# Kernel tuning notes

Measured on AMD Instinct MI355X. Metric: run time of the kernel, lower is better.

Reference implementation:

```python
import jax, jax.numpy as jnp
import numpy as np

N_NODES = 100000
N_EDGES = 400000
N_GRAPHS = 4096
F_IN, HID, HEADS, OUT_DIM = 64, 64, 4, 128
NEG_SLOPE = 0.2


def gat_layer(x, src, dst, W, a_s, a_d, b, concat):
    # x: [N, Fin]; W: [Fin, H*C]; a_s/a_d: [H, C]; src/dst: [Etot] (self loops included)
    N = x.shape[0]
    H, C = a_s.shape
    h = (x @ W).reshape(N, H, C)
    e_src = jnp.einsum('nhc,hc->nh', h, a_s)  # [N, H]
    e_dst = jnp.einsum('nhc,hc->nh', h, a_d)
    e = jax.nn.leaky_relu(e_src[src] + e_dst[dst], NEG_SLOPE)  # [Etot, H]
    # segment softmax over edges grouped by destination node
    m = jax.ops.segment_max(e, dst, num_segments=N)
    m = jnp.where(jnp.isfinite(m), m, 0.0)
    ex = jnp.exp(e - m[dst])
    denom = jax.ops.segment_sum(ex, dst, num_segments=N)
    alpha = ex / jnp.maximum(denom[dst], 1e-16)  # [Etot, H]
    out = jax.ops.segment_sum(alpha[:, :, None] * h[src], dst, num_segments=N)  # [N, H, C]
    out = out.reshape(N, H * C) if concat else out.mean(axis=1)
    return out + b


def setup_inputs() -> dict:
    key = jax.random.key(0)
    ks = jax.random.split(key, 32)
    x = jax.random.normal(ks[0], (N_NODES, F_IN), dtype=jnp.float32)
    edge_index = jax.random.randint(ks[1], (2, N_EDGES), 0, N_NODES, dtype=jnp.int64) if jax.config.jax_enable_x64 else jax.random.randint(ks[1], (2, N_EDGES), 0, N_NODES).astype(jnp.int32)
    batch = jnp.sort(jax.random.randint(ks[2], (N_NODES,), 0, N_GRAPHS)).astype(edge_index.dtype)
    s = 0.1
    d = {
        'x': x, 'edge_index': edge_index, 'batch': batch, 'num_graphs': N_GRAPHS,
        'W0': jax.random.normal(ks[3], (F_IN, HEADS * HID), jnp.float32) * s,
        'as0': jax.random.normal(ks[4], (HEADS, HID), jnp.float32) * s,
        'ad0': jax.random.normal(ks[5], (HEADS, HID), jnp.float32) * s,
        'b0': jnp.zeros((HEADS * HID,), jnp.float32),
        'W1': jax.random.normal(ks[6], (HEADS * HID, HEADS * HID), jnp.float32) * s,
        'as1': jax.random.normal(ks[7], (HEADS, HID), jnp.float32) * s,
        'ad1': jax.random.normal(ks[8], (HEADS, HID), jnp.float32) * s,
        'b1': jnp.zeros((HEADS * HID,), jnp.float32),
        'W2': jax.random.normal(ks[9], (HEADS * HID, HEADS * HID), jnp.float32) * s,
        'as2': jax.random.normal(ks[10], (HEADS, HID), jnp.float32) * s,
        'ad2': jax.random.normal(ks[11], (HEADS, HID), jnp.float32) * s,
        'b2': jnp.zeros((HEADS * HID,), jnp.float32),
        'W3': jax.random.normal(ks[12], (HEADS * HID, OUT_DIM), jnp.float32) * s,
        'as3': jax.random.normal(ks[13], (1, OUT_DIM), jnp.float32) * s,
        'ad3': jax.random.normal(ks[14], (1, OUT_DIM), jnp.float32) * s,
        'b3': jnp.zeros((OUT_DIM,), jnp.float32),
        'mW0': jax.random.normal(ks[15], (OUT_DIM, OUT_DIM // 2), jnp.float32) * s,
        'mb0': jnp.zeros((OUT_DIM // 2,), jnp.float32),
        'mW1': jax.random.normal(ks[16], (OUT_DIM // 2, OUT_DIM // 4), jnp.float32) * s,
        'mb1': jnp.zeros((OUT_DIM // 4,), jnp.float32),
        'mW2': jax.random.normal(ks[17], (OUT_DIM // 4, 4), jnp.float32) * s,
        'mb2': jnp.zeros((4,), jnp.float32),
    }
    return d


def reference(x, edge_index, batch, num_graphs, W0, as0, ad0, b0, W1, as1, ad1, b1,
              W2, as2, ad2, b2, W3, as3, ad3, b3, mW0, mb0, mW1, mb1, mW2, mb2):
    N = x.shape[0]
    # PyG GATConv default add_self_loops=True
    loop = jnp.arange(N, dtype=edge_index.dtype)
    src = jnp.concatenate([edge_index[0], loop])
    dst = jnp.concatenate([edge_index[1], loop])
    # dropout layers are identity in eval mode
    h = gat_layer(x, src, dst, W0, as0, ad0, b0, concat=True)
    h = jax.nn.elu(h)
    h = gat_layer(h, src, dst, W1, as1, ad1, b1, concat=True)
    h = jax.nn.elu(h)
    h = gat_layer(h, src, dst, W2, as2, ad2, b2, concat=True)
    h = jax.nn.elu(h)
    h = gat_layer(h, src, dst, W3, as3, ad3, b3, concat=False)  # [N, OUT_DIM]
    # global mean pool per graph
    sums = jax.ops.segment_sum(h, batch, num_segments=num_graphs)
    cnt = jax.ops.segment_sum(jnp.ones((N,), h.dtype), batch, num_segments=num_graphs)
    pooled = sums / jnp.maximum(cnt, 1.0)[:, None]  # [G, OUT_DIM]
    # MLPReadout(out_dim, 4, L=2): 128 -> 64 -> 32 -> 4 with ReLU between
    y = jax.nn.relu(pooled @ mW0 + mb0)
    y = jax.nn.relu(y @ mW1 + mb1)
    y = y @ mW2 + mb2
    return y
```

## Files before the change

### kernel.cpp

```cpp
#include <hip/hip_runtime.h>
#include <math.h>

#define N_NODES 100000
#define N_EDGES 400000
#define N_GRAPHS_C 4096
#define E_TOT (N_EDGES + N_NODES)

static inline int ceil_div(int a, int b) { return (a + b - 1) / b; }

typedef __attribute__((ext_vector_type(8))) short short8v;
typedef __attribute__((ext_vector_type(4))) float float4v;

#define GLL16(g, l)                                                                          \
  __builtin_amdgcn_global_load_lds((const __attribute__((address_space(1))) unsigned int*)(g), \
                                   (__attribute__((address_space(3))) unsigned int*)(l), 16, 0, 0)

__device__ __forceinline__ float b2f(unsigned short u) {
  union { unsigned int i; float f; } v;
  v.i = ((unsigned int)u) << 16;
  return v.f;
}
__device__ __forceinline__ unsigned short f2b(float f) {
  union { float f; unsigned int i; } v;
  v.f = f;
  unsigned int x = v.i;
  unsigned int r = x + 0x7fffu + ((x >> 16) & 1u);
  return (unsigned short)(r >> 16);
}


__global__ __launch_bounds__(256) void k_cvt_x(const float* __restrict__ in, unsigned short* __restrict__ out,
                                               int n4) {
  int i = blockIdx.x * 256 + threadIdx.x;
  if (i >= n4) return;
  float4 v = *(const float4*)(in + (size_t)i * 4);
  ushort4 o;
  o.x = f2b(v.x); o.y = f2b(v.y); o.z = f2b(v.z); o.w = f2b(v.w);
  *(ushort4*)(out + (size_t)i * 4) = o;
}

__device__ __forceinline__ void cvt_one(const float* __restrict__ W, unsigned short* __restrict__ Wt,
                                        int K, int Ncol, int idx) {
  int n = idx / K, k = idx % K;
  Wt[(size_t)n * K + k] = f2b(W[(size_t)k * Ncol + n]);
}

__global__ __launch_bounds__(256) void k_cvt_w_all(const float* __restrict__ W0, unsigned short* __restrict__ wt0,
                                                   const float* __restrict__ W1, unsigned short* __restrict__ wt1,
                                                   const float* __restrict__ W2, unsigned short* __restrict__ wt2,
                                                   const float* __restrict__ W3, unsigned short* __restrict__ wt3) {
  int i = blockIdx.x * 256 + threadIdx.x;
  const int s0 = 64 * 256, s1 = s0 + 256 * 256, s2 = s1 + 256 * 256, s3 = s2 + 256 * 128;
  if (i < s0) cvt_one(W0, wt0, 64, 256, i);
  else if (i < s1) cvt_one(W1, wt1, 256, 256, i - s0);
  else if (i < s2) cvt_one(W2, wt2, 256, 256, i - s1);
  else if (i < s3) cvt_one(W3, wt3, 256, 128, i - s2);
}

__device__ __forceinline__ void wa_one(const float* __restrict__ W, const float* __restrict__ a_s,
                                       const float* __restrict__ a_d, unsigned short* __restrict__ wt,
                                       int K, int Ncol, int H, int C, int idx) {
  int k = idx % K;
  int j = idx / K;
  const float* a = (j < H) ? a_s : a_d;
  int h = (j < H) ? j : j - H;
  float s = 0.f;
  for (int c = 0; c < C; c++) s += W[(size_t)k * Ncol + h * C + c] * a[h * C + c];
  wt[(size_t)(Ncol + j) * K + k] = f2b(s);
}

__global__ __launch_bounds__(256) void k_cvt_wa(const float* __restrict__ W0, const float* __restrict__ as0, const float* __restrict__ ad0, unsigned short* __restrict__ wt0,
                                                const float* __restrict__ W1, const float* __restrict__ as1, const float* __restrict__ ad1, unsigned short* __restrict__ wt1,
                                                const float* __restrict__ W2, const float* __restrict__ as2, const float* __restrict__ ad2, unsigned short* __restrict__ wt2,
                                                const float* __restrict__ W3, const float* __restrict__ as3, const float* __restrict__ ad3, unsigned short* __restrict__ wt3) {
  int i = blockIdx.x * 256 + threadIdx.x;
  const int s0 = 64 * 8, s1 = s0 + 256 * 8, s2 = s1 + 256 * 8, s3 = s2 + 256 * 2;
  if (i < s0) wa_one(W0, as0, ad0, wt0, 64, 256, 4, 64, i);
  else if (i < s1) wa_one(W1, as1, ad1, wt1, 256, 256, 4, 64, i - s0);
  else if (i < s2) wa_one(W2, as2, ad2, wt2, 256, 256, 4, 64, i - s1);
  else if (i < s3) wa_one(W3, as3, ad3, wt3, 256, 128, 1, 128, i - s2);
}


__global__ __launch_bounds__(256) void k_count_deg_g(const int* __restrict__ ei, int* __restrict__ deg,
                                                     const int* __restrict__ batch, int* __restrict__ gcnt) {
  int i = blockIdx.x * 256 + threadIdx.x;
  if (i < N_EDGES) atomicAdd(&deg[ei[N_EDGES + i]], 1);
  if (i < N_NODES) atomicAdd(&gcnt[batch[i]], 1);
}

__global__ __launch_bounds__(256) void k_scan(int* __restrict__ deg, int* __restrict__ offs,
                                              int* __restrict__ cursor, int* __restrict__ counter) {
  __shared__ int sm[256];
  __shared__ int sbase;
  int tid = threadIdx.x;
  int n = blockIdx.x * 256 + tid;
  int d = (n < N_NODES) ? (deg[n] + 1) : 0;
  sm[tid] = d;
  __syncthreads();
  for (int off = 1; off < 256; off <<= 1) {
    int v = (tid >= off) ? sm[tid - off] : 0;
    __syncthreads();
    sm[tid] += v;
    __syncthreads();
  }
  if (tid == 255) sbase = atomicAdd(counter, sm[255]);
  __syncthreads();
  int excl = sm[tid] - d;
  if (n < N_NODES) {
    int o = sbase + excl;
    offs[n] = o;
    cursor[n] = o;
    deg[n] = d;
  }
}

__global__ __launch_bounds__(256) void k_scatter(const int* __restrict__ ei, int* __restrict__ cursor,
                                                 int* __restrict__ csr) {
  int i = blockIdx.x * 256 + threadIdx.x;
  if (i < N_EDGES) {
    int d = ei[N_EDGES + i];
    int pos = atomicAdd(&cursor[d], 1);
    csr[pos] = ei[i];
  } else if (i < E_TOT) {
    int n = i - N_EDGES;
    int pos = atomicAdd(&cursor[n], 1);
    csr[pos] = n;
  }
}

__global__ __launch_bounds__(256) void k_gscan(const int* __restrict__ gcnt, int* __restrict__ gptr) {
  __shared__ int sm[256];
  __shared__ int srun;
  int tid = threadIdx.x;
  if (tid == 0) srun = 0;
  __syncthreads();
  for (int c = 0; c < N_GRAPHS_C / 256; c++) {
    int idx = c * 256 + tid;
    int v = gcnt[idx];
    sm[tid] = v;
    __syncthreads();
    for (int off = 1; off < 256; off <<= 1) {
      int t = (tid >= off) ? sm[tid - off] : 0;
      __syncthreads();
      sm[tid] += t;
      __syncthreads();
    }
    gptr[idx] = srun + sm[tid] - v;
    __syncthreads();
    if (tid == 0) srun += sm[255];
    __syncthreads();
  }
}


template <int ATT>
__global__ __launch_bounds__(256) void k_gemm_bf16(const unsigned short* __restrict__ A,
                                                   const unsigned short* __restrict__ Wt,
                                                   unsigned short* __restrict__ out, int M, int K, int Ncol,
                                                   float* __restrict__ es, float* __restrict__ ed) {
  __shared__ unsigned short As[128 * 32];
  __shared__ unsigned short Bs[144 * 32];
  int tid = threadIdx.x;
  int wave = tid >> 6, lane = tid & 63;
  int quad = lane >> 4, l16 = lane & 15;
  int wrow = (wave & 1) * 64, wcol = (wave >> 1) * 64;
  int row0 = blockIdx.x * 128, col0 = blockIdx.y * 128;

  constexpr int EX = (ATT == 1) ? 8 : 2;
  bool blockExtra = (ATT == 1) ? (blockIdx.y == 1) : true;

  float4v acc[4][4];
#pragma unroll
  for (int i = 0; i < 4; i++)
#pragma unroll
    for (int j = 0; j < 4; j++) acc[i][j] = (float4v)(0.f);
  float4v acc_e[4];
#pragma unroll
  for (int i = 0; i < 4; i++) acc_e[i] = (float4v)(0.f);

  int lrow = lane >> 2;
  int lcb = (lane & 3) * 8;
  int ca = wave, cb = wave + 4;

  for (int k0 = 0; k0 < K; k0 += 32) {
    GLL16(A + (size_t)(row0 + ca * 16 + lrow) * K + k0 + lcb, &As[ca * 512]);
    GLL16(A + (size_t)(row0 + cb * 16 + lrow) * K + k0 + lcb, &As[cb * 512]);
    GLL16(Wt + (size_t)(col0 + ca * 16 + lrow) * K + k0 + lcb, &Bs[ca * 512]);
    GLL16(Wt + (size_t)(col0 + cb * 16 + lrow) * K + k0 + lcb, &Bs[cb * 512]);
    if (blockExtra && wave == 0)
      GLL16(Wt + (size_t)(Ncol + lrow) * K + k0 + lcb, &Bs[8 * 512]);
    __syncthreads();

    short8v af[4], bf[4];
#pragma unroll
    for (int i = 0; i < 4; i++)
      af[i] = *(const short8v*)(&As[(wrow + i * 16 + l16) * 32 + quad * 8]);
#pragma unroll
    for (int j = 0; j < 4; j++)
      bf[j] = *(const short8v*)(&Bs[(wcol + j * 16 + l16) * 32 + quad * 8]);
#pragma unroll
    for (int i = 0; i < 4; i++)
#pragma unroll
      for (int j = 0; j < 4; j++)
        acc[i][j] = __builtin_amdgcn_mfma_f32_16x16x32_bf16(af[i], bf[j], acc[i][j], 0, 0, 0);
    if (blockExtra && wcol == 0) {
      short8v bfe = *(const short8v*)(&Bs[(128 + l16) * 32 + quad * 8]);
#pragma unroll
      for (int i = 0; i < 4; i++)
        acc_e[i] = __builtin_amdgcn_mfma_f32_16x16x32_bf16(af[i], bfe, acc_e[i], 0, 0, 0);
    }
    __syncthreads();
  }

#pragma unroll
  for (int i = 0; i < 4; i++) {
#pragma unroll
    for (int r = 0; r < 4; r++) {
      int m = row0 + wrow + i * 16 + quad * 4 + r;
      if (m < M) {
#pragma unroll
        for (int j = 0; j < 4; j++) {
          int col = col0 + wcol + j * 16 + l16;
          out[(size_t)m * Ncol + col] = f2b(acc[i][j][r]);
        }
      }
    }
  }

  if (blockExtra && wcol == 0 && l16 < EX) {
    constexpr int H = (ATT == 1) ? 4 : 1;
    float* dst = (l16 < H) ? es : ed;
    int h = (l16 < H) ? l16 : l16 - H;
#pragma unroll
    for (int i = 0; i < 4; i++) {
#pragma unroll
      for (int r = 0; r < 4; r++) {
        int m = row0 + wrow + i * 16 + quad * 4 + r;
        if (m < M) dst[m * H + h] = acc_e[i][r];
      }
    }
  }
}


template <int H>
__global__ __launch_bounds__(256) void k_logits_node(const float* __restrict__ es, const float* __restrict__ ed,
                                                     const int* __restrict__ csr, const int* __restrict__ offs,
                                                     const int* __restrict__ deg, float* __restrict__ ew,
                                                     float* __restrict__ inv) {
  int n = blockIdx.x * 256 + threadIdx.x;
  if (n >= N_NODES) return;
  int start = offs[n];
  int c = deg[n];
  const int* csrp = csr + start;
  if (H == 4) {
    float4 edn = *(const float4*)(ed + (size_t)n * 4);
    float s0 = 0.f, s1 = 0.f, s2 = 0.f, s3 = 0.f;
    for (int i = 0; i < c; i++) {
      int s = csrp[i];
      float4 a = *(const float4*)(es + (size_t)s * 4);
      float e0 = a.x + edn.x; e0 = e0 > 0.f ? e0 : 0.2f * e0; e0 = __expf(e0);
      float e1 = a.y + edn.y; e1 = e1 > 0.f ? e1 : 0.2f * e1; e1 = __expf(e1);
      float e2 = a.z + edn.z; e2 = e2 > 0.f ? e2 : 0.2f * e2; e2 = __expf(e2);
      float e3 = a.w + edn.w; e3 = e3 > 0.f ? e3 : 0.2f * e3; e3 = __expf(e3);
      *(float4*)(ew + ((size_t)start + i) * 4) = make_float4(e0, e1, e2, e3);
      s0 += e0; s1 += e1; s2 += e2; s3 += e3;
    }
    float4 iv;
    iv.x = 1.0f / fmaxf(s0, 1e-16f);
    iv.y = 1.0f / fmaxf(s1, 1e-16f);
    iv.z = 1.0f / fmaxf(s2, 1e-16f);
    iv.w = 1.0f / fmaxf(s3, 1e-16f);
    *(float4*)(inv + (size_t)n * 4) = iv;
  } else {
    float edn = ed[n];
    float sum = 0.f;
    for (int i = 0; i < c; i++) {
      int s = csrp[i];
      float e = es[s] + edn;
      e = e > 0.f ? e : 0.2f * e;
      e = __expf(e);
      ew[start + i] = e;
      sum += e;
    }
    inv[n] = 1.0f / fmaxf(sum, 1e-16f);
  }
}


__device__ __forceinline__ void acc4(float* acc, float w, uint2 u) {
  acc[0] += w * b2f((unsigned short)(u.x & 0xffff));
  acc[1] += w * b2f((unsigned short)(u.x >> 16));
  acc[2] += w * b2f((unsigned short)(u.y & 0xffff));
  acc[3] += w * b2f((unsigned short)(u.y >> 16));
}
__device__ __forceinline__ void acc2(float* acc, float w, unsigned int u) {
  acc[0] += w * b2f((unsigned short)(u & 0xffff));
  acc[1] += w * b2f((unsigned short)(u >> 16));
}

template <int H, int C>
__global__ __launch_bounds__(256) void k_aggregate(const unsigned short* __restrict__ hbuf,
                                                   const float* __restrict__ ew, const float* __restrict__ inv,
                                                   const int* __restrict__ offs, const int* __restrict__ deg,
                                                   const int* __restrict__ csr, const float* __restrict__ bias,
                                                   unsigned short* __restrict__ out, int applyElu) {
  constexpr int F = H * C;
  constexpr int VPL = F / 64;
  int wave = threadIdx.x >> 6;
  int lane = threadIdx.x & 63;
  int n = blockIdx.x * 4 + wave;
  if (n >= N_NODES) return;
  int head = (H == 1) ? 0 : (lane >> 4);
  int start = offs[n];
  int cnt = deg[n];
  const float* ewp = ew + (size_t)start * H + head;
  const int* csrp = csr + start;

  float acc[VPL];
#pragma unroll
  for (int j = 0; j < VPL; j++) acc[j] = 0.f;

  int i = 0;
  for (; i + 4 <= cnt; i += 4) {
    int s0 = csrp[i], s1 = csrp[i + 1], s2 = csrp[i + 2], s3 = csrp[i + 3];
    float w0 = ewp[(size_t)(i + 0) * H];
    float w1 = ewp[(size_t)(i + 1) * H];
    float w2 = ewp[(size_t)(i + 2) * H];
    float w3 = ewp[(size_t)(i + 3) * H];
    if (VPL == 4) {
      uint2 u0 = *(const uint2*)(hbuf + (size_t)s0 * F + lane * 4);
      uint2 u1 = *(const uint2*)(hbuf + (size_t)s1 * F + lane * 4);
      uint2 u2 = *(const uint2*)(hbuf + (size_t)s2 * F + lane * 4);
      uint2 u3 = *(const uint2*)(hbuf + (size_t)s3 * F + lane * 4);
      acc4(acc, w0, u0); acc4(acc, w1, u1); acc4(acc, w2, u2); acc4(acc, w3, u3);
    } else {
      unsigned int u0 = *(const unsigned int*)(hbuf + (size_t)s0 * F + lane * 2);
      unsigned int u1 = *(const unsigned int*)(hbuf + (size_t)s1 * F + lane * 2);
      unsigned int u2 = *(const unsigned int*)(hbuf + (size_t)s2 * F + lane * 2);
      unsigned int u3 = *(const unsigned int*)(hbuf + (size_t)s3 * F + lane * 2);
      acc2(acc, w0, u0); acc2(acc, w1, u1); acc2(acc, w2, u2); acc2(acc, w3, u3);
    }
  }
  for (; i < cnt; i++) {
    int s = csrp[i];
    float w = ewp[(size_t)i * H];
    if (VPL == 4) {
      uint2 u = *(const uint2*)(hbuf + (size_t)s * F + lane * 4);
      acc4(acc, w, u);
    } else {
      unsigned int u = *(const unsigned int*)(hbuf + (size_t)s * F + lane * 2);
      acc2(acc, w, u);
    }
  }

  float iv = inv[n * H + head];
  unsigned short ob[VPL];
#pragma unroll
  for (int j = 0; j < VPL; j++) {
    float v = acc[j] * iv + bias[lane * VPL + j];
    if (applyElu) v = v > 0.f ? v : expm1f(v);
    ob[j] = f2b(v);
  }
  if (VPL == 4) {
    ushort4 o = make_ushort4(ob[0], ob[1], ob[2], ob[3]);
    *(ushort4*)(out + (size_t)n * F + lane * 4) = o;
  } else {
    ushort2 o = make_ushort2(ob[0], ob[1]);
    *(ushort2*)(out + (size_t)n * F + lane * 2) = o;
  }
}


__global__ __launch_bounds__(128) void k_pool_readout(const unsigned short* __restrict__ feat,
                                                      const int* __restrict__ gptr, const int* __restrict__ gcnt,
                                                      const float* __restrict__ mW0, const float* __restrict__ mb0,
                                                      const float* __restrict__ mW1, const float* __restrict__ mb1,
                                                      const float* __restrict__ mW2, const float* __restrict__ mb2,
                                                      float* __restrict__ out) {
  __shared__ float part[2][128];
  __shared__ float p[128];
  __shared__ float y1[64];
  __shared__ float y2[32];
  int g = blockIdx.x;
  int t = threadIdx.x;
  int w = t >> 6, lane = t & 63;
  int start = gptr[g];
  int c = gcnt[g];
  float a0 = 0.f, a1 = 0.f;
  for (int i = w; i < c; i += 2) {
    unsigned int u = *(const unsigned int*)(feat + (size_t)(start + i) * 128 + lane * 2);
    a0 += b2f((unsigned short)(u & 0xffff));
    a1 += b2f((unsigned short)(u >> 16));
  }
  part[w][lane * 2 + 0] = a0;
  part[w][lane * 2 + 1] = a1;
  __syncthreads();
  float invc = 1.0f / fmaxf((float)c, 1.0f);
  p[t] = (part[0][t] + part[1][t]) * invc;
  __syncthreads();
  if (t < 64) {
    float v = mb0[t];
#pragma unroll 4
    for (int k = 0; k < 128; k++) v += p[k] * mW0[k * 64 + t];
    y1[t] = v > 0.f ? v : 0.f;
  }
  __syncthreads();
  if (t < 32) {
    float v = mb1[t];
#pragma unroll 4
    for (int k = 0; k < 64; k++) v += y1[k] * mW1[k * 32 + t];
    y2[t] = v > 0.f ? v : 0.f;
  }
  __syncthreads();
  if (t < 4) {
    float v = mb2[t];
#pragma unroll 4
    for (int k = 0; k < 32; k++) v += y2[k] * mW2[k * 4 + t];
    out[(size_t)g * 4 + t] = v;
  }
}


extern "C" void kernel_launch(void* const* d_in, const int* in_sizes, int n_in,
                              void* d_out, int out_size, void* d_ws, size_t ws_size,
                              hipStream_t stream) {
  const float* x = (const float*)d_in[0];
  const int* ei = (const int*)d_in[1];
  const int* batch = (const int*)d_in[2];
  const float* W0 = (const float*)d_in[4];
  const float* as0 = (const float*)d_in[5];
  const float* ad0 = (const float*)d_in[6];
  const float* b0 = (const float*)d_in[7];
  const float* W1 = (const float*)d_in[8];
  const float* as1 = (const float*)d_in[9];
  const float* ad1 = (const float*)d_in[10];
  const float* b1 = (const float*)d_in[11];
  const float* W2 = (const float*)d_in[12];
  const float* as2 = (const float*)d_in[13];
  const float* ad2 = (const float*)d_in[14];
  const float* b2 = (const float*)d_in[15];
  const float* W3 = (const float*)d_in[16];
  const float* as3 = (const float*)d_in[17];
  const float* ad3 = (const float*)d_in[18];
  const float* b3 = (const float*)d_in[19];
  const float* mW0 = (const float*)d_in[20];
  const float* mb0 = (const float*)d_in[21];
  const float* mW1 = (const float*)d_in[22];
  const float* mb1 = (const float*)d_in[23];
  const float* mW2 = (const float*)d_in[24];
  const float* mb2 = (const float*)d_in[25];
  float* out = (float*)d_out;

  char* ws = (char*)d_ws;
  size_t cur = 0;
  auto alloc = [&](size_t bytes) -> char* {
    char* p = ws + cur;
    cur += (bytes + 255) & ~(size_t)255;
    return p;
  };
  unsigned short* featA = (unsigned short*)alloc((size_t)N_NODES * 256 * 2);
  unsigned short* hB = (unsigned short*)alloc((size_t)N_NODES * 256 * 2);
  unsigned short* xb = (unsigned short*)alloc((size_t)N_NODES * 64 * 2);
  unsigned short* wt0 = (unsigned short*)alloc((size_t)272 * 64 * 2);
  unsigned short* wt1 = (unsigned short*)alloc((size_t)272 * 256 * 2);
  unsigned short* wt2 = (unsigned short*)alloc((size_t)272 * 256 * 2);
  unsigned short* wt3 = (unsigned short*)alloc((size_t)144 * 256 * 2);
  float* es = (float*)alloc((size_t)N_NODES * 4 * sizeof(float));
  float* ed = (float*)alloc((size_t)N_NODES * 4 * sizeof(float));
  float* ew = (float*)alloc((size_t)E_TOT * 4 * sizeof(float));
  float* inv = (float*)alloc((size_t)N_NODES * 4 * sizeof(float));
  int* deg = (int*)alloc((size_t)N_NODES * sizeof(int));
  int* counter = (int*)alloc(256);
  int* gcnt = (int*)alloc((size_t)N_GRAPHS_C * sizeof(int));
  size_t zeroBytes = (char*)(gcnt + N_GRAPHS_C) - (char*)deg;
  int* offs = (int*)alloc((size_t)N_NODES * sizeof(int));
  int* cursor = (int*)alloc((size_t)N_NODES * sizeof(int));
  int* csr = (int*)alloc((size_t)E_TOT * sizeof(int));
  int* gptr = (int*)alloc((size_t)N_GRAPHS_C * sizeof(int));
  (void)alloc(128 * 1024);
  (void)ws_size; (void)in_sizes; (void)n_in; (void)out_size;

  k_cvt_x<<<ceil_div(N_NODES * 64 / 4, 256), 256, 0, stream>>>(x, xb, N_NODES * 64 / 4);
  k_cvt_w_all<<<ceil_div(64 * 256 + 2 * 256 * 256 + 256 * 128, 256), 256, 0, stream>>>(W0, wt0, W1, wt1, W2, wt2, W3, wt3);
  k_cvt_wa<<<ceil_div(64 * 8 + 2 * 256 * 8 + 256 * 2, 256), 256, 0, stream>>>(
      W0, as0, ad0, wt0, W1, as1, ad1, wt1, W2, as2, ad2, wt2, W3, as3, ad3, wt3);

  hipMemsetAsync(deg, 0, zeroBytes, stream);
  k_count_deg_g<<<ceil_div(N_EDGES, 256), 256, 0, stream>>>(ei, deg, batch, gcnt);
  k_scan<<<ceil_div(N_NODES, 256), 256, 0, stream>>>(deg, offs, cursor, counter);
  k_scatter<<<ceil_div(E_TOT, 256), 256, 0, stream>>>(ei, cursor, csr);
  k_gscan<<<1, 256, 0, stream>>>(gcnt, gptr);

  int gm = ceil_div(N_NODES, 128);
  dim3 g256(gm, 2), g128(gm, 1);
  int aggBlocks = ceil_div(N_NODES, 4);
  int nodeBlocks = ceil_div(N_NODES, 256);

  k_gemm_bf16<1><<<g256, 256, 0, stream>>>(xb, wt0, hB, N_NODES, 64, 256, es, ed);
  k_logits_node<4><<<nodeBlocks, 256, 0, stream>>>(es, ed, csr, offs, deg, ew, inv);
  k_aggregate<4, 64><<<aggBlocks, 256, 0, stream>>>(hB, ew, inv, offs, deg, csr, b0, featA, 1);

  k_gemm_bf16<1><<<g256, 256, 0, stream>>>(featA, wt1, hB, N_NODES, 256, 256, es, ed);
  k_logits_node<4><<<nodeBlocks, 256, 0, stream>>>(es, ed, csr, offs, deg, ew, inv);
  k_aggregate<4, 64><<<aggBlocks, 256, 0, stream>>>(hB, ew, inv, offs, deg, csr, b1, featA, 1);

  k_gemm_bf16<1><<<g256, 256, 0, stream>>>(featA, wt2, hB, N_NODES, 256, 256, es, ed);
  k_logits_node<4><<<nodeBlocks, 256, 0, stream>>>(es, ed, csr, offs, deg, ew, inv);
  k_aggregate<4, 64><<<aggBlocks, 256, 0, stream>>>(hB, ew, inv, offs, deg, csr, b2, featA, 1);

  k_gemm_bf16<2><<<g128, 256, 0, stream>>>(featA, wt3, hB, N_NODES, 256, 128, es, ed);
  k_logits_node<1><<<nodeBlocks, 256, 0, stream>>>(es, ed, csr, offs, deg, ew, inv);
  k_aggregate<1, 128><<<aggBlocks, 256, 0, stream>>>(hB, ew, inv, offs, deg, csr, b3, featA, 0);

  k_pool_readout<<<N_GRAPHS_C, 128, 0, stream>>>(featA, gptr, gcnt, mW0, mb0, mW1, mb1, mW2, mb2, out);
}
```

Measured before the change: 612.4 us.

## Compute attention logits per edge and fold softmax denominator into aggregation

Attention logits were computed by a per-node loop over incoming edges, which also summed the softmax denominator. They are now computed by one thread per CSR edge, with a new csr_dst array written during scatter. The denominator is accumulated inside the aggregate kernel from the weights it already reads. This removes the serial per-node loop and its degree imbalance, and drops the inv buffer. The three conversion kernels are also merged into a single launch. The cost is an extra destination-index array, with its writes in scatter and reads in every logits pass.

Result: faster. 592.3 us (-3.3%).

```diff
diff --git a/kernel.cpp b/kernel.cpp
--- a/kernel.cpp
+++ b/kernel.cpp
@@ -29,32 +29,10 @@
 }
 
 
-__global__ __launch_bounds__(256) void k_cvt_x(const float* __restrict__ in, unsigned short* __restrict__ out,
-                                               int n4) {
-  int i = blockIdx.x * 256 + threadIdx.x;
-  if (i >= n4) return;
-  float4 v = *(const float4*)(in + (size_t)i * 4);
-  ushort4 o;
-  o.x = f2b(v.x); o.y = f2b(v.y); o.z = f2b(v.z); o.w = f2b(v.w);
-  *(ushort4*)(out + (size_t)i * 4) = o;
-}
-
 __device__ __forceinline__ void cvt_one(const float* __restrict__ W, unsigned short* __restrict__ Wt,
                                         int K, int Ncol, int idx) {
   int n = idx / K, k = idx % K;
   Wt[(size_t)n * K + k] = f2b(W[(size_t)k * Ncol + n]);
-}
-
-__global__ __launch_bounds__(256) void k_cvt_w_all(const float* __restrict__ W0, unsigned short* __restrict__ wt0,
-                                                   const float* __restrict__ W1, unsigned short* __restrict__ wt1,
-                                                   const float* __restrict__ W2, unsigned short* __restrict__ wt2,
-                                                   const float* __restrict__ W3, unsigned short* __restrict__ wt3) {
-  int i = blockIdx.x * 256 + threadIdx.x;
-  const int s0 = 64 * 256, s1 = s0 + 256 * 256, s2 = s1 + 256 * 256, s3 = s2 + 256 * 128;
-  if (i < s0) cvt_one(W0, wt0, 64, 256, i);
-  else if (i < s1) cvt_one(W1, wt1, 256, 256, i - s0);
-  else if (i < s2) cvt_one(W2, wt2, 256, 256, i - s1);
-  else if (i < s3) cvt_one(W3, wt3, 256, 128, i - s2);
 }
 
 __device__ __forceinline__ void wa_one(const float* __restrict__ W, const float* __restrict__ a_s,
@@ -69,16 +47,35 @@
   wt[(size_t)(Ncol + j) * K + k] = f2b(s);
 }
 
-__global__ __launch_bounds__(256) void k_cvt_wa(const float* __restrict__ W0, const float* __restrict__ as0, const float* __restrict__ ad0, unsigned short* __restrict__ wt0,
-                                                const float* __restrict__ W1, const float* __restrict__ as1, const float* __restrict__ ad1, unsigned short* __restrict__ wt1,
-                                                const float* __restrict__ W2, const float* __restrict__ as2, const float* __restrict__ ad2, unsigned short* __restrict__ wt2,
-                                                const float* __restrict__ W3, const float* __restrict__ as3, const float* __restrict__ ad3, unsigned short* __restrict__ wt3) {
+__global__ __launch_bounds__(256) void k_cvt_all(
+    const float* __restrict__ x, unsigned short* __restrict__ xb,
+    const float* __restrict__ W0, const float* __restrict__ as0, const float* __restrict__ ad0, unsigned short* __restrict__ wt0,
+    const float* __restrict__ W1, const float* __restrict__ as1, const float* __restrict__ ad1, unsigned short* __restrict__ wt1,
+    const float* __restrict__ W2, const float* __restrict__ as2, const float* __restrict__ ad2, unsigned short* __restrict__ wt2,
+    const float* __restrict__ W3, const float* __restrict__ as3, const float* __restrict__ ad3, unsigned short* __restrict__ wt3) {
   int i = blockIdx.x * 256 + threadIdx.x;
-  const int s0 = 64 * 8, s1 = s0 + 256 * 8, s2 = s1 + 256 * 8, s3 = s2 + 256 * 2;
-  if (i < s0) wa_one(W0, as0, ad0, wt0, 64, 256, 4, 64, i);
-  else if (i < s1) wa_one(W1, as1, ad1, wt1, 256, 256, 4, 64, i - s0);
-  else if (i < s2) wa_one(W2, as2, ad2, wt2, 256, 256, 4, 64, i - s1);
-  else if (i < s3) wa_one(W3, as3, ad3, wt3, 256, 128, 1, 128, i - s2);
+  const int nx = N_NODES * 64 / 4;
+  const int w0e = nx + 64 * 256;
+  const int w1e = w0e + 256 * 256;
+  const int w2e = w1e + 256 * 256;
+  const int w3e = w2e + 256 * 128;
+  const int a0e = w3e + 64 * 8;
+  const int a1e = a0e + 256 * 8;
+  const int a2e = a1e + 256 * 8;
+  const int a3e = a2e + 256 * 2;
+  if (i < nx) {
+    float4 v = *(const float4*)(x + (size_t)i * 4);
+    ushort4 o;
+    o.x = f2b(v.x); o.y = f2b(v.y); o.z = f2b(v.z); o.w = f2b(v.w);
+    *(ushort4*)(xb + (size_t)i * 4) = o;
+  } else if (i < w0e) cvt_one(W0, wt0, 64, 256, i - nx);
+  else if (i < w1e) cvt_one(W1, wt1, 256, 256, i - w0e);
+  else if (i < w2e) cvt_one(W2, wt2, 256, 256, i - w1e);
+  else if (i < w3e) cvt_one(W3, wt3, 256, 128, i - w2e);
+  else if (i < a0e) wa_one(W0, as0, ad0, wt0, 64, 256, 4, 64, i - w3e);
+  else if (i < a1e) wa_one(W1, as1, ad1, wt1, 256, 256, 4, 64, i - a0e);
+  else if (i < a2e) wa_one(W2, as2, ad2, wt2, 256, 256, 4, 64, i - a1e);
+  else if (i < a3e) wa_one(W3, as3, ad3, wt3, 256, 128, 1, 128, i - a2e);
 }
 
 
@@ -116,16 +113,18 @@
 }
 
 __global__ __launch_bounds__(256) void k_scatter(const int* __restrict__ ei, int* __restrict__ cursor,
-                                                 int* __restrict__ csr) {
+                                                 int* __restrict__ csr, int* __restrict__ csr_dst) {
   int i = blockIdx.x * 256 + threadIdx.x;
   if (i < N_EDGES) {
     int d = ei[N_EDGES + i];
     int pos = atomicAdd(&cursor[d], 1);
     csr[pos] = ei[i];
+    csr_dst[pos] = d;
   } else if (i < E_TOT) {
     int n = i - N_EDGES;
     int pos = atomicAdd(&cursor[n], 1);
     csr[pos] = n;
+    csr_dst[pos] = n;
   }
 }
 
@@ -245,46 +244,24 @@
 
 
 template <int H>
-__global__ __launch_bounds__(256) void k_logits_node(const float* __restrict__ es, const float* __restrict__ ed,
-                                                     const int* __restrict__ csr, const int* __restrict__ offs,
-                                                     const int* __restrict__ deg, float* __restrict__ ew,
-                                                     float* __restrict__ inv) {
-  int n = blockIdx.x * 256 + threadIdx.x;
-  if (n >= N_NODES) return;
-  int start = offs[n];
-  int c = deg[n];
-  const int* csrp = csr + start;
+__global__ __launch_bounds__(256) void k_logits_edge(const float* __restrict__ es, const float* __restrict__ ed,
+                                                     const int* __restrict__ csr, const int* __restrict__ csr_dst,
+                                                     float* __restrict__ ew) {
+  int p = blockIdx.x * 256 + threadIdx.x;
+  if (p >= E_TOT) return;
+  int s = csr[p], d = csr_dst[p];
   if (H == 4) {
-    float4 edn = *(const float4*)(ed + (size_t)n * 4);
-    float s0 = 0.f, s1 = 0.f, s2 = 0.f, s3 = 0.f;
-    for (int i = 0; i < c; i++) {
-      int s = csrp[i];
-      float4 a = *(const float4*)(es + (size_t)s * 4);
-      float e0 = a.x + edn.x; e0 = e0 > 0.f ? e0 : 0.2f * e0; e0 = __expf(e0);
-      float e1 = a.y + edn.y; e1 = e1 > 0.f ? e1 : 0.2f * e1; e1 = __expf(e1);
-      float e2 = a.z + edn.z; e2 = e2 > 0.f ? e2 : 0.2f * e2; e2 = __expf(e2);
-      float e3 = a.w + edn.w; e3 = e3 > 0.f ? e3 : 0.2f * e3; e3 = __expf(e3);
-      *(float4*)(ew + ((size_t)start + i) * 4) = make_float4(e0, e1, e2, e3);
-      s0 += e0; s1 += e1; s2 += e2; s3 += e3;
-    }
-    float4 iv;
-    iv.x = 1.0f / fmaxf(s0, 1e-16f);
-    iv.y = 1.0f / fmaxf(s1, 1e-16f);
-    iv.z = 1.0f / fmaxf(s2, 1e-16f);
-    iv.w = 1.0f / fmaxf(s3, 1e-16f);
-    *(float4*)(inv + (size_t)n * 4) = iv;
+    float4 a = *(const float4*)(es + (size_t)s * 4);
+    float4 b = *(const float4*)(ed + (size_t)d * 4);
+    float e0 = a.x + b.x; e0 = e0 > 0.f ? e0 : 0.2f * e0; e0 = __expf(e0);
+    float e1 = a.y + b.y; e1 = e1 > 0.f ? e1 : 0.2f * e1; e1 = __expf(e1);
+    float e2 = a.z + b.z; e2 = e2 > 0.f ? e2 : 0.2f * e2; e2 = __expf(e2);
+    float e3 = a.w + b.w; e3 = e3 > 0.f ? e3 : 0.2f * e3; e3 = __expf(e3);
+    *(float4*)(ew + (size_t)p * 4) = make_float4(e0, e1, e2, e3);
   } else {
-    float edn = ed[n];
-    float sum = 0.f;
-    for (int i = 0; i < c; i++) {
-      int s = csrp[i];
-      float e = es[s] + edn;
-      e = e > 0.f ? e : 0.2f * e;
-      e = __expf(e);
-      ew[start + i] = e;
-      sum += e;
-    }
-    inv[n] = 1.0f / fmaxf(sum, 1e-16f);
+    float e = es[s] + ed[d];
+    e = e > 0.f ? e : 0.2f * e;
+    ew[p] = __expf(e);
   }
 }
 
@@ -302,7 +279,7 @@
 
 template <int H, int C>
 __global__ __launch_bounds__(256) void k_aggregate(const unsigned short* __restrict__ hbuf,
-                                                   const float* __restrict__ ew, const float* __restrict__ inv,
+                                                   const float* __restrict__ ew,
                                                    const int* __restrict__ offs, const int* __restrict__ deg,
                                                    const int* __restrict__ csr, const float* __restrict__ bias,
                                                    unsigned short* __restrict__ out, int applyElu) {
@@ -321,6 +298,7 @@
   float acc[VPL];
 #pragma unroll
   for (int j = 0; j < VPL; j++) acc[j] = 0.f;
+  float dsum = 0.f;
 
   int i = 0;
   for (; i + 4 <= cnt; i += 4) {
@@ -329,6 +307,7 @@
     float w1 = ewp[(size_t)(i + 1) * H];
     float w2 = ewp[(size_t)(i + 2) * H];
     float w3 = ewp[(size_t)(i + 3) * H];
+    dsum += (w0 + w1) + (w2 + w3);
     if (VPL == 4) {
       uint2 u0 = *(const uint2*)(hbuf + (size_t)s0 * F + lane * 4);
       uint2 u1 = *(const uint2*)(hbuf + (size_t)s1 * F + lane * 4);
@@ -346,6 +325,7 @@
   for (; i < cnt; i++) {
     int s = csrp[i];
     float w = ewp[(size_t)i * H];
+    dsum += w;
     if (VPL == 4) {
       uint2 u = *(const uint2*)(hbuf + (size_t)s * F + lane * 4);
       acc4(acc, w, u);
@@ -355,7 +335,7 @@
     }
   }
 
-  float iv = inv[n * H + head];
+  float iv = 1.0f / fmaxf(dsum, 1e-16f);
   unsigned short ob[VPL];
 #pragma unroll
   for (int j = 0; j < VPL; j++) {
@@ -470,7 +450,6 @@
   float* es = (float*)alloc((size_t)N_NODES * 4 * sizeof(float));
   float* ed = (float*)alloc((size_t)N_NODES * 4 * sizeof(float));
   float* ew = (float*)alloc((size_t)E_TOT * 4 * sizeof(float));
-  float* inv = (float*)alloc((size_t)N_NODES * 4 * sizeof(float));
   int* deg = (int*)alloc((size_t)N_NODES * sizeof(int));
   int* counter = (int*)alloc(256);
   int* gcnt = (int*)alloc((size_t)N_GRAPHS_C * sizeof(int));
@@ -478,41 +457,42 @@
   int* offs = (int*)alloc((size_t)N_NODES * sizeof(int));
   int* cursor = (int*)alloc((size_t)N_NODES * sizeof(int));
   int* csr = (int*)alloc((size_t)E_TOT * sizeof(int));
+  int* csr_dst = (int*)alloc((size_t)E_TOT * sizeof(int));
   int* gptr = (int*)alloc((size_t)N_GRAPHS_C * sizeof(int));
   (void)alloc(128 * 1024);
   (void)ws_size; (void)in_sizes; (void)n_in; (void)out_size;
 
-  k_cvt_x<<<ceil_div(N_NODES * 64 / 4, 256), 256, 0, stream>>>(x, xb, N_NODES * 64 / 4);
-  k_cvt_w_all<<<ceil_div(64 * 256 + 2 * 256 * 256 + 256 * 128, 256), 256, 0, stream>>>(W0, wt0, W1, wt1, W2, wt2, W3, wt3);
-  k_cvt_wa<<<ceil_div(64 * 8 + 2 * 256 * 8 + 256 * 2, 256), 256, 0, stream>>>(
-      W0, as0, ad0, wt0, W1, as1, ad1, wt1, W2, as2, ad2, wt2, W3, as3, ad3, wt3);
+  const int cvtTotal = N_NODES * 64 / 4 + 64 * 256 + 2 * 256 * 256 + 256 * 128 +
+                       64 * 8 + 2 * 256 * 8 + 256 * 2;
+  k_cvt_all<<<ceil_div(cvtTotal, 256), 256, 0, stream>>>(
+      x, xb, W0, as0, ad0, wt0, W1, as1, ad1, wt1, W2, as2, ad2, wt2, W3, as3, ad3, wt3);
 
   hipMemsetAsync(deg, 0, zeroBytes, stream);
   k_count_deg_g<<<ceil_div(N_EDGES, 256), 256, 0, stream>>>(ei, deg, batch, gcnt);
   k_scan<<<ceil_div(N_NODES, 256), 256, 0, stream>>>(deg, offs, cursor, counter);
-  k_scatter<<<ceil_div(E_TOT, 256), 256, 0, stream>>>(ei, cursor, csr);
+  k_scatter<<<ceil_div(E_TOT, 256), 256, 0, stream>>>(ei, cursor, csr, csr_dst);
   k_gscan<<<1, 256, 0, stream>>>(gcnt, gptr);
 
   int gm = ceil_div(N_NODES, 128);
   dim3 g256(gm, 2), g128(gm, 1);
   int aggBlocks = ceil_div(N_NODES, 4);
-  int nodeBlocks = ceil_div(N_NODES, 256);
+  int edgeBlocks = ceil_div(E_TOT, 256);
 
   k_gemm_bf16<1><<<g256, 256, 0, stream>>>(xb, wt0, hB, N_NODES, 64, 256, es, ed);
-  k_logits_node<4><<<nodeBlocks, 256, 0, stream>>>(es, ed, csr, offs, deg, ew, inv);
-  k_aggregate<4, 64><<<aggBlocks, 256, 0, stream>>>(hB, ew, inv, offs, deg, csr, b0, featA, 1);
+  k_logits_edge<4><<<edgeBlocks, 256, 0, stream>>>(es, ed, csr, csr_dst, ew);
+  k_aggregate<4, 64><<<aggBlocks, 256, 0, stream>>>(hB, ew, offs, deg, csr, b0, featA, 1);
 
   k_gemm_bf16<1><<<g256, 256, 0, stream>>>(featA, wt1, hB, N_NODES, 256, 256, es, ed);
-  k_logits_node<4><<<nodeBlocks, 256, 0, stream>>>(es, ed, csr, offs, deg, ew, inv);
-  k_aggregate<4, 64><<<aggBlocks, 256, 0, stream>>>(hB, ew, inv, offs, deg, csr, b1, featA, 1);
+  k_logits_edge<4><<<edgeBlocks, 256, 0, stream>>>(es, ed, csr, csr_dst, ew);
+  k_aggregate<4, 64><<<aggBlocks, 256, 0, stream>>>(hB, ew, offs, deg, csr, b1, featA, 1);
 
   k_gemm_bf16<1><<<g256, 256, 0, stream>>>(featA, wt2, hB, N_NODES, 256, 256, es, ed);
-  k_logits_node<4><<<nodeBlocks, 256, 0, stream>>>(es, ed, csr, offs, deg, ew, inv);
-  k_aggregate<4, 64><<<aggBlocks, 256, 0, stream>>>(hB, ew, inv, offs, deg, csr, b2, featA, 1);
+  k_logits_edge<4><<<edgeBlocks, 256, 0, stream>>>(es, ed, csr, csr_dst, ew);
+  k_aggregate<4, 64><<<aggBlocks, 256, 0, stream>>>(hB, ew, offs, deg, csr, b2, featA, 1);
 
   k_gemm_bf16<2><<<g128, 256, 0, stream>>>(featA, wt3, hB, N_NODES, 256, 128, es, ed);
-  k_logits_node<1><<<nodeBlocks, 256, 0, stream>>>(es, ed, csr, offs, deg, ew, inv);
-  k_aggregate<1, 128><<<aggBlocks, 256, 0, stream>>>(hB, ew, inv, offs, deg, csr, b3, featA, 0);
+  k_logits_edge<1><<<edgeBlocks, 256, 0, stream>>>(es, ed, csr, csr_dst, ew);
+  k_aggregate<1, 128><<<aggBlocks, 256, 0, stream>>>(hB, ew, offs, deg, csr, b3, featA, 0);
 
   k_pool_readout<<<N_GRAPHS_C, 128, 0, stream>>>(featA, gptr, gcnt, mW0, mb0, mW1, mb1, mW2, mb2, out);
 }
```
